# Performance work log

Measured on AMD Instinct MI355X. Metric: run time of the kernel, lower is better.

Reference implementation:

```python
import jax, jax.numpy as jnp
import numpy as np

# MiniCPM3 MLA attention dims
HIDDEN = 2560
N_HEADS = 40
Q_LORA = 768
KV_LORA = 256
ROPE_D = 32
NOPE_D = 64
V_D = HIDDEN // N_HEADS          # 64
Q_HEAD_D = NOPE_D + ROPE_D       # 96
ROPE_BASE = 10000.0
EPS = 1e-6


def setup_inputs() -> dict:
    key = jax.random.key(0)
    ks = jax.random.split(key, 8)
    B, S = 1, 2048
    sc = lambda fan_in: 1.0 / np.sqrt(fan_in)
    return {
        "hidden_states": jax.random.normal(ks[0], (B, S, HIDDEN), jnp.float32),
        "position_ids": jnp.arange(B * S, dtype=jnp.int64).reshape(B, S) % S,
        "w_qa": jax.random.normal(ks[1], (HIDDEN, Q_LORA), jnp.float32) * sc(HIDDEN),
        "q_a_ln_w": jnp.ones((Q_LORA,), jnp.float32),
        "w_qb": jax.random.normal(ks[2], (Q_LORA, N_HEADS * Q_HEAD_D), jnp.float32) * sc(Q_LORA),
        "w_kva": jax.random.normal(ks[3], (HIDDEN, KV_LORA + ROPE_D), jnp.float32) * sc(HIDDEN),
        "kv_a_ln_w": jnp.ones((KV_LORA,), jnp.float32),
        "w_kvb": jax.random.normal(ks[4], (KV_LORA, N_HEADS * (NOPE_D + V_D)), jnp.float32) * sc(KV_LORA),
        "w_o": jax.random.normal(ks[5], (N_HEADS * V_D, HIDDEN), jnp.float32) * sc(N_HEADS * V_D),
    }


def _rmsnorm(x, w, eps=EPS):
    var = jnp.mean(x * x, axis=-1, keepdims=True)
    return x * jax.lax.rsqrt(var + eps) * w


def _rotate_half(x):
    h = x.shape[-1] // 2
    return jnp.concatenate([-x[..., h:], x[..., :h]], axis=-1)


def _rope_cache(seq_len, dim, base, dtype=jnp.float32):
    inv_freq = 1.0 / (base ** (jnp.arange(0, dim, 2, dtype=jnp.float32) / dim))
    t = jnp.arange(seq_len, dtype=jnp.float32)
    freqs = jnp.outer(t, inv_freq)                      # [S, dim/2]
    emb = jnp.concatenate([freqs, freqs], axis=-1)      # [S, dim]
    return jnp.cos(emb).astype(dtype), jnp.sin(emb).astype(dtype)


def reference(hidden_states, position_ids, w_qa, q_a_ln_w, w_qb, w_kva, kv_a_ln_w, w_kvb, w_o):
    B, S, _ = hidden_states.shape
    # --- low-rank Q projection: a -> RMSNorm -> b ---
    q = _rmsnorm(hidden_states @ w_qa, q_a_ln_w) @ w_qb          # [B,S,H*96]
    q = q.reshape(B, S, N_HEADS, Q_HEAD_D).transpose(0, 2, 1, 3)  # [B,H,S,96]
    q_nope, q_pe = q[..., :NOPE_D], q[..., NOPE_D:]
    # --- compressed KV + shared rope key ---
    ckv = hidden_states @ w_kva                                   # [B,S,256+32]
    compressed_kv, k_pe = ckv[..., :KV_LORA], ckv[..., KV_LORA:]
    k_pe = k_pe[:, None, :, :]                                    # [B,1,S,32]
    kv = _rmsnorm(compressed_kv, kv_a_ln_w) @ w_kvb               # [B,S,H*(64+64)]
    kv = kv.reshape(B, S, N_HEADS, NOPE_D + V_D).transpose(0, 2, 1, 3)
    k_nope, v = kv[..., :NOPE_D], kv[..., NOPE_D:]                # [B,H,S,64] each
    # --- RoPE on the 32-dim rope sub-dimension (fp32, as original) ---
    cos, sin = _rope_cache(S, ROPE_D, ROPE_BASE)
    cos = cos[position_ids][:, None, :, :]                        # [B,1,S,32]
    sin = sin[position_ids][:, None, :, :]
    q_pe = q_pe * cos + _rotate_half(q_pe) * sin
    k_pe = k_pe * cos + _rotate_half(k_pe) * sin
    # --- concat nope/rope parts ---
    q_full = jnp.concatenate([q_nope, q_pe], axis=-1)             # [B,H,S,96]
    k_full = jnp.concatenate([k_nope, jnp.broadcast_to(k_pe, (B, N_HEADS, S, ROPE_D))], axis=-1)
    # --- causal SDPA with scale q_head_dim**-0.5 ---
    scale = Q_HEAD_D ** -0.5
    scores = jnp.einsum("bhqd,bhkd->bhqk", q_full, k_full) * scale
    causal = jnp.tril(jnp.ones((S, S), bool))
    scores = jnp.where(causal, scores, jnp.finfo(scores.dtype).min)
    probs = jax.nn.softmax(scores, axis=-1)
    attn = jnp.einsum("bhqk,bhkd->bhqd", probs, v)                # [B,H,S,64]
    attn = attn.transpose(0, 2, 1, 3).reshape(B, S, N_HEADS * V_D)
    return attn @ w_o
```

## Files before the change

kernel.cpp:

```cpp
#include <hip/hip_runtime.h>
#include <hip/hip_bf16.h>

typedef __hip_bfloat16 bf16;
typedef __attribute__((ext_vector_type(8))) __bf16 bf16x8;
typedef __attribute__((ext_vector_type(4))) __bf16 bf16x4;
typedef __attribute__((ext_vector_type(4))) float f32x4;

constexpr int S_LEN = 2048;
constexpr int HID   = 2560;
constexpr int NH    = 40;
constexpr int QL    = 768;
constexpr int KVL   = 256;
constexpr int RD    = 32;
constexpr int ND    = 64;
constexpr int VD    = 64;
constexpr int QHD   = 96;
constexpr int QB_N  = NH * QHD;
constexpr int KVB_N = NH * (ND + VD);
constexpr int CKV_N = KVL + RD;
constexpr int AB_N  = QL + CKV_N;

#define MFMA16(a, b, c) __builtin_amdgcn_mfma_f32_16x16x32_bf16((a), (b), (c), 0, 0, 0)

__device__ __forceinline__ int get_pos(const int* pos, int s) {
  bool is64 = (pos[1] == 0 && pos[2] == 1);
  return is64 ? pos[2 * s] : pos[s];
}


__global__ void cast_f32_bf16(const float* __restrict__ src, bf16* __restrict__ dst, int n4) {
  int i = blockIdx.x * blockDim.x + threadIdx.x;
  if (i >= n4) return;
  float4 v = reinterpret_cast<const float4*>(src)[i];
  struct { bf16 a, b, c, d; } pk;
  pk.a = __float2bfloat16(v.x); pk.b = __float2bfloat16(v.y);
  pk.c = __float2bfloat16(v.z); pk.d = __float2bfloat16(v.w);
  reinterpret_cast<uint2*>(dst)[i] = *reinterpret_cast<uint2*>(&pk);
}

__global__ void transpose_cast(const float* __restrict__ src, bf16* __restrict__ dst, int K, int N) {
  __shared__ float tile[32][33];
  int nb = blockIdx.x * 32, kb = blockIdx.y * 32;
  int x = threadIdx.x, y = threadIdx.y;
#pragma unroll
  for (int j = 0; j < 4; ++j) {
    int k = kb + y + j * 8, n = nb + x;
    tile[y + j * 8][x] = (k < K && n < N) ? src[(size_t)k * N + n] : 0.f;
  }
  __syncthreads();
#pragma unroll
  for (int j = 0; j < 4; ++j) {
    int n = nb + y + j * 8, k = kb + x;
    if (n < N && k < K) dst[(size_t)n * K + k] = __float2bfloat16(tile[x][y + j * 8]);
  }
}


__global__ __launch_bounds__(256) void gemm_qakva(const bf16* __restrict__ A,
                                                  const bf16* __restrict__ B,
                                                  float* __restrict__ q_out,
                                                  float* __restrict__ ckv_out) {
  constexpr int BM = 64, BK = 64, K = HID, N = AB_N;
  __shared__ __bf16 ldsA[BM * BK];
  __shared__ __bf16 ldsB[64 * BK];
  const int t = threadIdx.x;
  const int l = t & 63, w = t >> 6;
  const int lr = l & 15, lk = l >> 4;
  const int rowbase = blockIdx.y * BM;
  const int colbase = blockIdx.x * 64;

  f32x4 acc[4];
#pragma unroll
  for (int n = 0; n < 4; ++n) acc[n] = f32x4{0.f, 0.f, 0.f, 0.f};

  for (int kt = 0; kt < K / BK; ++kt) {
    const int kb = kt * BK;
#pragma unroll
    for (int it = 0; it < 2; ++it) {
      const int r  = it * 32 + w * 8 + (l >> 3);
      const int c8 = ((l & 7) * 8) ^ ((r & 7) << 3);
      const bf16* ga = A + (size_t)(rowbase + r) * K + kb + c8;
      __builtin_amdgcn_global_load_lds((const __attribute__((address_space(1))) void*)ga,
          (__attribute__((address_space(3))) void*)(ldsA + it * 2048 + w * 512), 16, 0, 0);
      int nrow = colbase + r;
      nrow = (nrow < N) ? nrow : (N - 1);
      const bf16* gb = B + (size_t)nrow * K + kb + c8;
      __builtin_amdgcn_global_load_lds((const __attribute__((address_space(1))) void*)gb,
          (__attribute__((address_space(3))) void*)(ldsB + it * 2048 + w * 512), 16, 0, 0);
    }
    __syncthreads();
#pragma unroll
    for (int kk = 0; kk < 2; ++kk) {
      const int arow = w * 16 + lr;
      const int ace  = (kk * 32 + lk * 8) ^ ((arow & 7) << 3);
      bf16x8 af = *(const bf16x8*)(ldsA + arow * BK + ace);
#pragma unroll
      for (int n = 0; n < 4; ++n) {
        const int row = n * 16 + lr;
        const int ce  = (kk * 32 + lk * 8) ^ ((row & 7) << 3);
        bf16x8 bfr = *(const bf16x8*)(ldsB + row * BK + ce);
        acc[n] = MFMA16(af, bfr, acc[n]);
      }
    }
    __syncthreads();
  }

#pragma unroll
  for (int n = 0; n < 4; ++n) {
    const int col = colbase + n * 16 + lr;
#pragma unroll
    for (int i = 0; i < 4; ++i) {
      const int row = rowbase + w * 16 + lk * 4 + i;
      if (col < QL)       q_out[(size_t)row * QL + col] = acc[n][i];
      else if (col < N)   ckv_out[(size_t)row * CKV_N + (col - QL)] = acc[n][i];
    }
  }
}

__global__ __launch_bounds__(256) void gemm_out64(const bf16* __restrict__ A,
                                                  const bf16* __restrict__ B,
                                                  float* __restrict__ C) {
  constexpr int BM = 128, BK = 64, K = HID, N = HID;
  __shared__ __bf16 ldsA[BM * BK];
  __shared__ __bf16 ldsB[64 * BK];
  const int t = threadIdx.x;
  const int l = t & 63, w = t >> 6;
  const int lr = l & 15, lk = l >> 4;
  const int rowbase = blockIdx.y * BM;
  const int colbase = blockIdx.x * 64;

  f32x4 acc[2][4];
#pragma unroll
  for (int m = 0; m < 2; ++m)
#pragma unroll
    for (int n = 0; n < 4; ++n) acc[m][n] = f32x4{0.f, 0.f, 0.f, 0.f};

  for (int kt = 0; kt < K / BK; ++kt) {
    const int kb = kt * BK;
#pragma unroll
    for (int it = 0; it < 4; ++it) {
      const int r  = it * 32 + w * 8 + (l >> 3);
      const int c8 = ((l & 7) * 8) ^ ((r & 7) << 3);
      const bf16* ga = A + (size_t)(rowbase + r) * K + kb + c8;
      __builtin_amdgcn_global_load_lds((const __attribute__((address_space(1))) void*)ga,
          (__attribute__((address_space(3))) void*)(ldsA + it * 2048 + w * 512), 16, 0, 0);
      if (it < 2) {
        const bf16* gb = B + (size_t)(colbase + r) * K + kb + c8;
        __builtin_amdgcn_global_load_lds((const __attribute__((address_space(1))) void*)gb,
            (__attribute__((address_space(3))) void*)(ldsB + it * 2048 + w * 512), 16, 0, 0);
      }
    }
    __syncthreads();
#pragma unroll
    for (int kk = 0; kk < 2; ++kk) {
      bf16x8 af[2], bfr[4];
#pragma unroll
      for (int m = 0; m < 2; ++m) {
        const int row = w * 32 + m * 16 + lr;
        const int ce  = (kk * 32 + lk * 8) ^ ((row & 7) << 3);
        af[m] = *(const bf16x8*)(ldsA + row * BK + ce);
      }
#pragma unroll
      for (int n = 0; n < 4; ++n) {
        const int row = n * 16 + lr;
        const int ce  = (kk * 32 + lk * 8) ^ ((row & 7) << 3);
        bfr[n] = *(const bf16x8*)(ldsB + row * BK + ce);
      }
#pragma unroll
      for (int m = 0; m < 2; ++m)
#pragma unroll
        for (int n = 0; n < 4; ++n)
          acc[m][n] = MFMA16(af[m], bfr[n], acc[m][n]);
    }
    __syncthreads();
  }

#pragma unroll
  for (int m = 0; m < 2; ++m)
#pragma unroll
    for (int n = 0; n < 4; ++n) {
      const int col = colbase + n * 16 + lr;
#pragma unroll
      for (int i = 0; i < 4; ++i) {
        const int row = rowbase + w * 32 + m * 16 + lk * 4 + i;
        C[(size_t)row * N + col] = acc[m][n][i];
      }
    }
}

__global__ __launch_bounds__(256) void gemm_qb_rope(const bf16* __restrict__ A,
                                                    const bf16* __restrict__ B,
                                                    const float* __restrict__ ropc,
                                                    const float* __restrict__ rops,
                                                    bf16* __restrict__ qfull) {
  constexpr int BM = 128, BK = 64, K = QL;
  __shared__ __bf16 ldsA[BM * BK];
  __shared__ __bf16 ldsB[64 * BK];
  const int t = threadIdx.x;
  const int l = t & 63, w = t >> 6;
  const int lr = l & 15, lk = l >> 4;
  const int rowbase = blockIdx.y * BM;
  const int colbase = blockIdx.x * 64;
  const float scale = 0.14724444f;

  f32x4 acc[2][4];
#pragma unroll
  for (int m = 0; m < 2; ++m)
#pragma unroll
    for (int n = 0; n < 4; ++n) acc[m][n] = f32x4{0.f, 0.f, 0.f, 0.f};

  for (int kt = 0; kt < K / BK; ++kt) {
    const int kb = kt * BK;
#pragma unroll
    for (int it = 0; it < 4; ++it) {
      const int r  = it * 32 + w * 8 + (l >> 3);
      const int c8 = ((l & 7) * 8) ^ ((r & 7) << 3);
      const bf16* ga = A + (size_t)(rowbase + r) * K + kb + c8;
      __builtin_amdgcn_global_load_lds((const __attribute__((address_space(1))) void*)ga,
          (__attribute__((address_space(3))) void*)(ldsA + it * 2048 + w * 512), 16, 0, 0);
      if (it < 2) {
        const bf16* gb = B + (size_t)(colbase + r) * K + kb + c8;
        __builtin_amdgcn_global_load_lds((const __attribute__((address_space(1))) void*)gb,
            (__attribute__((address_space(3))) void*)(ldsB + it * 2048 + w * 512), 16, 0, 0);
      }
    }
    __syncthreads();
#pragma unroll
    for (int kk = 0; kk < 2; ++kk) {
      bf16x8 af[2], bfr[4];
#pragma unroll
      for (int m = 0; m < 2; ++m) {
        const int row = w * 32 + m * 16 + lr;
        const int ce  = (kk * 32 + lk * 8) ^ ((row & 7) << 3);
        af[m] = *(const bf16x8*)(ldsA + row * BK + ce);
      }
#pragma unroll
      for (int n = 0; n < 4; ++n) {
        const int row = n * 16 + lr;
        const int ce  = (kk * 32 + lk * 8) ^ ((row & 7) << 3);
        bfr[n] = *(const bf16x8*)(ldsB + row * BK + ce);
      }
#pragma unroll
      for (int m = 0; m < 2; ++m)
#pragma unroll
        for (int n = 0; n < 4; ++n)
          acc[m][n] = MFMA16(af[m], bfr[n], acc[m][n]);
    }
    __syncthreads();
  }

#pragma unroll
  for (int m = 0; m < 2; ++m) {
    const int rowtop = rowbase + w * 32 + m * 16 + lk * 4;
#pragma unroll
    for (int n = 0; n < 4; ++n) {
      const int c0 = colbase + n * 16;
      const int h  = c0 / 96;
      const int d0 = c0 - h * 96;
      const size_t qb_ = ((size_t)h * S_LEN + rowtop) * QHD + d0 + lr;
      if (d0 < ND) {
#pragma unroll
        for (int i = 0; i < 4; ++i)
          qfull[qb_ + (size_t)i * QHD] = __float2bfloat16(acc[m][n][i] * scale);
      } else if (d0 == ND) {
#pragma unroll
        for (int i = 0; i < 4; ++i) {
          const float c = ropc[(rowtop + i) * 16 + lr];
          const float s = rops[(rowtop + i) * 16 + lr];
          const float x0 = acc[m][n][i], x1 = acc[m][n + 1][i];
          qfull[qb_ + (size_t)i * QHD] = __float2bfloat16((x0 * c - x1 * s) * scale);
        }
      } else {
#pragma unroll
        for (int i = 0; i < 4; ++i) {
          const float c = ropc[(rowtop + i) * 16 + lr];
          const float s = rops[(rowtop + i) * 16 + lr];
          const float x1 = acc[m][n][i], x0 = acc[m][n - 1][i];
          qfull[qb_ + (size_t)i * QHD] = __float2bfloat16((x1 * c + x0 * s) * scale);
        }
      }
    }
  }
}

__global__ __launch_bounds__(256) void gemm_kvb_split(const bf16* __restrict__ A,
                                                      const bf16* __restrict__ B,
                                                      bf16* __restrict__ kfull,
                                                      bf16* __restrict__ vt) {
  constexpr int BM = 128, BN = 128, BK = 64, K = KVL;
  __shared__ __bf16 ldsA[BM * BK];
  __shared__ __bf16 ldsB[BN * BK];
  const int t = threadIdx.x;
  const int l = t & 63, w = t >> 6;
  const int lr = l & 15, lk = l >> 4;
  const int wr = w >> 1, wc = w & 1;
  const int rowbase = blockIdx.y * BM;
  const int h = blockIdx.x;
  const int colbase = h * BN;

  f32x4 acc[4][4];
#pragma unroll
  for (int m = 0; m < 4; ++m)
#pragma unroll
    for (int n = 0; n < 4; ++n) acc[m][n] = f32x4{0.f, 0.f, 0.f, 0.f};

  for (int kt = 0; kt < K / BK; ++kt) {
    const int kb = kt * BK;
#pragma unroll
    for (int it = 0; it < 4; ++it) {
      const int r  = it * 32 + w * 8 + (l >> 3);
      const int c8 = ((l & 7) * 8) ^ ((r & 7) << 3);
      const bf16* ga = A + (size_t)(rowbase + r) * K + kb + c8;
      __builtin_amdgcn_global_load_lds((const __attribute__((address_space(1))) void*)ga,
          (__attribute__((address_space(3))) void*)(ldsA + it * 2048 + w * 512), 16, 0, 0);
      const bf16* gb = B + (size_t)(colbase + r) * K + kb + c8;
      __builtin_amdgcn_global_load_lds((const __attribute__((address_space(1))) void*)gb,
          (__attribute__((address_space(3))) void*)(ldsB + it * 2048 + w * 512), 16, 0, 0);
    }
    __syncthreads();
#pragma unroll
    for (int kk = 0; kk < 2; ++kk) {
      bf16x8 af[4], bfr[4];
#pragma unroll
      for (int m = 0; m < 4; ++m) {
        const int row = wr * 64 + m * 16 + lr;
        const int ce  = (kk * 32 + lk * 8) ^ ((row & 7) << 3);
        af[m] = *(const bf16x8*)(ldsA + row * BK + ce);
      }
#pragma unroll
      for (int n = 0; n < 4; ++n) {
        const int row = wc * 64 + n * 16 + lr;
        const int ce  = (kk * 32 + lk * 8) ^ ((row & 7) << 3);
        bfr[n] = *(const bf16x8*)(ldsB + row * BK + ce);
      }
#pragma unroll
      for (int m = 0; m < 4; ++m)
#pragma unroll
        for (int n = 0; n < 4; ++n)
          acc[m][n] = MFMA16(af[m], bfr[n], acc[m][n]);
    }
    __syncthreads();
  }

#pragma unroll
  for (int m = 0; m < 4; ++m) {
    const int rowtop = rowbase + wr * 64 + m * 16 + lk * 4;
    if (wc == 0) {
#pragma unroll
      for (int n = 0; n < 4; ++n) {
        const int d = n * 16 + lr;
#pragma unroll
        for (int i = 0; i < 4; ++i)
          kfull[((size_t)h * S_LEN + rowtop + i) * QHD + d] = __float2bfloat16(acc[m][n][i]);
      }
    } else {
#pragma unroll
      for (int n = 0; n < 4; ++n) {
        const int d = n * 16 + lr;
        bf16x4 pk;
#pragma unroll
        for (int i = 0; i < 4; ++i) pk[i] = (__bf16)acc[m][n][i];
        *(bf16x4*)(vt + ((size_t)h * VD + d) * S_LEN + rowtop) = pk;
      }
    }
  }
}


__global__ void rmsnorm_rows(const float* __restrict__ in, const float* __restrict__ w,
                             bf16* __restrict__ out, int C) {
  const int r = blockIdx.x;
  const float* row = in + (size_t)r * C;
  float ss = 0.f;
  for (int c = threadIdx.x; c < C; c += 256) { float v = row[c]; ss += v * v; }
#pragma unroll
  for (int d = 32; d > 0; d >>= 1) ss += __shfl_xor(ss, d);
  __shared__ float red[4];
  if ((threadIdx.x & 63) == 0) red[threadIdx.x >> 6] = ss;
  __syncthreads();
  const float tot = red[0] + red[1] + red[2] + red[3];
  const float rs = rsqrtf(tot / (float)C + 1e-6f);
  for (int c = threadIdx.x; c < C; c += 256)
    out[(size_t)r * C + c] = __float2bfloat16(row[c] * rs * w[c]);
}

__global__ void kv_prep(const float* __restrict__ ckv, const float* __restrict__ w,
                        const int* __restrict__ pos, bf16* __restrict__ ckv_bf,
                        bf16* __restrict__ kfull, float* __restrict__ ropc,
                        float* __restrict__ rops) {
  const int s = blockIdx.x, t = threadIdx.x;
  __shared__ bf16 pe_lds[32];
  const float* row = ckv + (size_t)s * CKV_N;
  float v[4]; float ss = 0.f;
#pragma unroll
  for (int j = 0; j < 4; ++j) { v[j] = row[t + 64 * j]; ss += v[j] * v[j]; }
#pragma unroll
  for (int d = 32; d > 0; d >>= 1) ss += __shfl_xor(ss, d);
  const float rs = rsqrtf(ss / (float)KVL + 1e-6f);
#pragma unroll
  for (int j = 0; j < 4; ++j)
    ckv_bf[(size_t)s * KVL + t + 64 * j] = __float2bfloat16(v[j] * rs * w[t + 64 * j]);
  if (t < 16) {
    const float x0 = row[KVL + t], x1 = row[KVL + 16 + t];
    const float p = (float)get_pos(pos, s);
    const float invf = exp2f(-(float)t * (13.2877124f / 16.f));
    const float ang = p * invf, c = cosf(ang), sn = sinf(ang);
    ropc[s * 16 + t] = c;
    rops[s * 16 + t] = sn;
    pe_lds[t]      = __float2bfloat16(x0 * c - x1 * sn);
    pe_lds[16 + t] = __float2bfloat16(x1 * c + x0 * sn);
  }
  __syncthreads();
  for (int idx = t; idx < NH * 32; idx += 64) {
    const int h = idx >> 5, d = idx & 31;
    kfull[((size_t)h * S_LEN + s) * QHD + ND + d] = pe_lds[d];
  }
}

__global__ __launch_bounds__(64) void attn_kernel(const bf16* __restrict__ qfull,
                                                  const bf16* __restrict__ kfull,
                                                  const bf16* __restrict__ vt,
                                                  bf16* __restrict__ ctx) {
  const int h = blockIdx.x;
  const int qw = ((int)gridDim.y - 1 - (int)blockIdx.y) * 32;
  const int l = threadIdx.x;
  const int lr = l & 15, lk = l >> 4;
  const bf16* Q  = qfull + (size_t)h * S_LEN * QHD;
  const bf16* Kf = kfull + (size_t)h * S_LEN * QHD;
  const bf16* V  = vt + (size_t)h * VD * S_LEN;
  __shared__ __bf16 plds[32][64];

  bf16x8 qf[2][3];
#pragma unroll
  for (int qg = 0; qg < 2; ++qg)
#pragma unroll
    for (int ks = 0; ks < 3; ++ks)
      qf[qg][ks] = *(const bf16x8*)(Q + (size_t)(qw + qg * 16 + lr) * QHD + ks * 32 + lk * 8);

  f32x4 o[2][4];
  float mrow[2], lrow[2];
#pragma unroll
  for (int qg = 0; qg < 2; ++qg) {
#pragma unroll
    for (int dt = 0; dt < 4; ++dt) o[qg][dt] = f32x4{0.f, 0.f, 0.f, 0.f};
    mrow[qg] = -1e30f; lrow[qg] = 0.f;
  }

  bf16x8 kf[4][3];
#pragma unroll
  for (int sub = 0; sub < 4; ++sub)
#pragma unroll
    for (int ks = 0; ks < 3; ++ks)
      kf[sub][ks] = *(const bf16x8*)(Kf + (size_t)(sub * 16 + lr) * QHD + ks * 32 + lk * 8);

  for (int kb = 0;; kb += 64) {
    bf16x8 vfr[2][4];
#pragma unroll
    for (int h2 = 0; h2 < 2; ++h2)
#pragma unroll
      for (int dt = 0; dt < 4; ++dt)
        vfr[h2][dt] = *(const bf16x8*)(V + (size_t)(dt * 16 + lr) * S_LEN + kb + h2 * 32 + lk * 8);

    f32x4 st[2][4];
#pragma unroll
    for (int qg = 0; qg < 2; ++qg)
#pragma unroll
      for (int sub = 0; sub < 4; ++sub) st[qg][sub] = f32x4{0.f, 0.f, 0.f, 0.f};
    __builtin_amdgcn_s_setprio(1);
#pragma unroll
    for (int qg = 0; qg < 2; ++qg)
#pragma unroll
      for (int sub = 0; sub < 4; ++sub)
#pragma unroll
        for (int ks = 0; ks < 3; ++ks)
          st[qg][sub] = MFMA16(kf[sub][ks], qf[qg][ks], st[qg][sub]);
    __builtin_amdgcn_s_setprio(0);

    const int nkb = kb + 64;
    if (nkb <= qw) {
#pragma unroll
      for (int sub = 0; sub < 4; ++sub)
#pragma unroll
        for (int ks = 0; ks < 3; ++ks)
          kf[sub][ks] = *(const bf16x8*)(Kf + (size_t)(nkb + sub * 16 + lr) * QHD + ks * 32 + lk * 8);
    }

    const bool diag = (kb + 64 > qw);
    float lmax[2];
#pragma unroll
    for (int qg = 0; qg < 2; ++qg) {
      const int q = qw + qg * 16 + lr;
      if (diag) {
#pragma unroll
        for (int sub = 0; sub < 4; ++sub)
#pragma unroll
          for (int i = 0; i < 4; ++i)
            if (kb + sub * 16 + lk * 4 + i > q) st[qg][sub][i] = -1e30f;
      }
      float m0 = -1e30f;
#pragma unroll
      for (int sub = 0; sub < 4; ++sub)
#pragma unroll
        for (int i = 0; i < 4; ++i) m0 = fmaxf(m0, st[qg][sub][i]);
      lmax[qg] = m0;
    }

    const bool noresc = __all((lmax[0] <= mrow[0] + 8.f) && (lmax[1] <= mrow[1] + 8.f));
    float mnew[2], fac[2];
    if (noresc) {
      mnew[0] = mrow[0]; mnew[1] = mrow[1];
    } else {
#pragma unroll
      for (int qg = 0; qg < 2; ++qg) {
        float t0 = lmax[qg];
        t0 = fmaxf(t0, __shfl_xor(t0, 16));
        t0 = fmaxf(t0, __shfl_xor(t0, 32));
        mnew[qg] = fmaxf(mrow[qg], t0);
        fac[qg] = exp2f(mrow[qg] - mnew[qg]);
        mrow[qg] = mnew[qg];
      }
    }

#pragma unroll
    for (int qg = 0; qg < 2; ++qg) {
      float ts = 0.f;
#pragma unroll
      for (int sub = 0; sub < 4; ++sub) {
        bf16x4 pk;
#pragma unroll
        for (int i = 0; i < 4; ++i) {
          const float p = exp2f(st[qg][sub][i] - mnew[qg]);
          ts += p;
          pk[i] = (__bf16)p;
        }
        const int swc = (sub * 16 + lk * 4) ^ ((lr & 7) << 3);
        *(bf16x4*)(&plds[qg * 16 + lr][swc]) = pk;
      }
      if (noresc) lrow[qg] += ts;
      else        lrow[qg] = lrow[qg] * fac[qg] + ts;
    }
    if (!noresc) {
#pragma unroll
      for (int qg = 0; qg < 2; ++qg)
#pragma unroll
        for (int i = 0; i < 4; ++i) {
          const float fr = __shfl(fac[qg], lk * 4 + i);
#pragma unroll
          for (int dt = 0; dt < 4; ++dt) o[qg][dt][i] *= fr;
        }
    }

#pragma unroll
    for (int h2 = 0; h2 < 2; ++h2) {
      const int swc = (h2 * 32 + lk * 8) ^ ((lr & 7) << 3);
      bf16x8 pa0 = *(const bf16x8*)(&plds[lr][swc]);
      bf16x8 pa1 = *(const bf16x8*)(&plds[16 + lr][swc]);
      __builtin_amdgcn_s_setprio(1);
#pragma unroll
      for (int dt = 0; dt < 4; ++dt) {
        o[0][dt] = MFMA16(pa0, vfr[h2][dt], o[0][dt]);
        o[1][dt] = MFMA16(pa1, vfr[h2][dt], o[1][dt]);
      }
      __builtin_amdgcn_s_setprio(0);
    }
    if (nkb > qw) break;
  }

#pragma unroll
  for (int qg = 0; qg < 2; ++qg) {
    float ls = lrow[qg];
    ls += __shfl_xor(ls, 16);
    ls += __shfl_xor(ls, 32);
    const float linv = 1.0f / ls;
#pragma unroll
    for (int i = 0; i < 4; ++i) {
      const float inv = __shfl(linv, lk * 4 + i);
#pragma unroll
      for (int dt = 0; dt < 4; ++dt) {
        const int row = qw + qg * 16 + lk * 4 + i;
        const int col = h * VD + dt * 16 + lr;
        ctx[(size_t)row * HID + col] = __float2bfloat16(o[qg][dt][i] * inv);
      }
    }
  }
}


extern "C" void kernel_launch(void* const* d_in, const int* in_sizes, int n_in,
                              void* d_out, int out_size, void* d_ws, size_t ws_size,
                              hipStream_t stream) {
  const float* hidden = (const float*)d_in[0];
  const int*   pos    = (const int*)d_in[1];
  const float* w_qa   = (const float*)d_in[2];
  const float* q_ln   = (const float*)d_in[3];
  const float* w_qb   = (const float*)d_in[4];
  const float* w_kva  = (const float*)d_in[5];
  const float* kv_ln  = (const float*)d_in[6];
  const float* w_kvb  = (const float*)d_in[7];
  const float* w_o    = (const float*)d_in[8];
  float* out = (float*)d_out;
  char* ws = (char*)d_ws;
  (void)in_sizes; (void)n_in; (void)out_size; (void)ws_size;

  size_t off = 0;
  auto take = [&](size_t bytes) -> char* {
    char* p = ws + off;
    off = (off + bytes + 255) & ~(size_t)255;
    return p;
  };
  bf16*  hid_bf = (bf16*)take((size_t)S_LEN * HID * 2);
  bf16*  wabT   = (bf16*)take((size_t)AB_N * HID * 2);
  bf16*  wqbT   = (bf16*)take((size_t)QB_N * QL * 2);
  bf16*  wkvbT  = (bf16*)take((size_t)KVB_N * KVL * 2);
  bf16*  woT    = (bf16*)take((size_t)HID * HID * 2);
  float* qlora  = (float*)take((size_t)S_LEN * QL * 4);
  bf16*  qa_bf  = (bf16*)take((size_t)S_LEN * QL * 2);
  bf16*  qfull  = (bf16*)take((size_t)NH * S_LEN * QHD * 2);
  float* ckv    = (float*)take((size_t)S_LEN * CKV_N * 4);
  bf16*  ckv_bf = (bf16*)take((size_t)S_LEN * KVL * 2);
  float* ropc   = (float*)take((size_t)S_LEN * 16 * 4);
  float* rops   = (float*)take((size_t)S_LEN * 16 * 4);
  bf16*  kfull  = (bf16*)take((size_t)NH * S_LEN * QHD * 2);
  bf16*  vt     = (bf16*)take((size_t)NH * VD * S_LEN * 2);
  bf16*  ctx    = (bf16*)take((size_t)S_LEN * HID * 2);

  const dim3 tb(32, 8);
  cast_f32_bf16<<<(S_LEN * HID / 4 + 255) / 256, 256, 0, stream>>>(hidden, hid_bf, S_LEN * HID / 4);
  transpose_cast<<<dim3((QL + 31) / 32, (HID + 31) / 32), tb, 0, stream>>>(w_qa, wabT, HID, QL);
  transpose_cast<<<dim3((CKV_N + 31) / 32, (HID + 31) / 32), tb, 0, stream>>>(w_kva, wabT + (size_t)QL * HID, HID, CKV_N);
  transpose_cast<<<dim3((QB_N + 31) / 32, (QL + 31) / 32), tb, 0, stream>>>(w_qb, wqbT, QL, QB_N);
  transpose_cast<<<dim3((KVB_N + 31) / 32, (KVL + 31) / 32), tb, 0, stream>>>(w_kvb, wkvbT, KVL, KVB_N);
  transpose_cast<<<dim3((HID + 31) / 32, (HID + 31) / 32), tb, 0, stream>>>(w_o, woT, HID, HID);

  gemm_qakva<<<dim3((AB_N + 63) / 64, S_LEN / 64), 256, 0, stream>>>(hid_bf, wabT, qlora, ckv);

  kv_prep<<<S_LEN, 64, 0, stream>>>(ckv, kv_ln, pos, ckv_bf, kfull, ropc, rops);

  rmsnorm_rows<<<S_LEN, 256, 0, stream>>>(qlora, q_ln, qa_bf, QL);
  gemm_qb_rope<<<dim3(QB_N / 64, S_LEN / 128), 256, 0, stream>>>(qa_bf, wqbT, ropc, rops, qfull);

  gemm_kvb_split<<<dim3(KVB_N / 128, S_LEN / 128), 256, 0, stream>>>(ckv_bf, wkvbT, kfull, vt);

  attn_kernel<<<dim3(NH, S_LEN / 32), 64, 0, stream>>>(qfull, kfull, vt, ctx);
  gemm_out64<<<dim3(HID / 64, S_LEN / 128), 256, 0, stream>>>(ctx, woT, out);
}
```

Measured before the change: 227.6 us.

## Split attention KV range across two waves with LDS softmax merge

Each attention block now runs two wavefronts. Each wave processes half of the causal KV tiles with its own online-softmax state, and the two partial results are merged through shared memory using max/sum rescaling. This is meant to shorten the serial KV loop per query tile and balance the causal workload, adding parallelism inside each block. The cost is extra LDS for the merge buffers, a barrier, and a merge epilogue. Query fragments are also loaded redundantly by both waves.

```diff
diff --git a/kernel.cpp b/kernel.cpp
--- a/kernel.cpp
+++ b/kernel.cpp
@@ -417,18 +417,27 @@
   }
 }
 
-__global__ __launch_bounds__(64) void attn_kernel(const bf16* __restrict__ qfull,
-                                                  const bf16* __restrict__ kfull,
-                                                  const bf16* __restrict__ vt,
-                                                  bf16* __restrict__ ctx) {
+__global__ __launch_bounds__(128) void attn_kernel(const bf16* __restrict__ qfull,
+                                                   const bf16* __restrict__ kfull,
+                                                   const bf16* __restrict__ vt,
+                                                   bf16* __restrict__ ctx) {
   const int h = blockIdx.x;
   const int qw = ((int)gridDim.y - 1 - (int)blockIdx.y) * 32;
-  const int l = threadIdx.x;
+  const int w = threadIdx.x >> 6;
+  const int l = threadIdx.x & 63;
   const int lr = l & 15, lk = l >> 4;
+  const int nt = (qw >> 6) + 1;
+  const int nA = (nt + 1) >> 1;
+  const int kb0    = (w == 0) ? 0 : nA * 64;
+  const int kbLast = (w == 0) ? (nA - 1) * 64 : (nt - 1) * 64;
+  const int diagkb = (nt - 1) * 64;
   const bf16* Q  = qfull + (size_t)h * S_LEN * QHD;
   const bf16* Kf = kfull + (size_t)h * S_LEN * QHD;
   const bf16* V  = vt + (size_t)h * VD * S_LEN;
-  __shared__ __bf16 plds[32][64];
+  __shared__ __bf16 plds[2][32][64];
+  __shared__ float cmbO[32][66];
+  __shared__ float lA_s[32];
+  __shared__ float mA_s[32];
 
   bf16x8 qf[2][3];
 #pragma unroll
@@ -446,140 +455,169 @@
     mrow[qg] = -1e30f; lrow[qg] = 0.f;
   }
 
-  bf16x8 kf[4][3];
-#pragma unroll
-  for (int sub = 0; sub < 4; ++sub)
-#pragma unroll
-    for (int ks = 0; ks < 3; ++ks)
-      kf[sub][ks] = *(const bf16x8*)(Kf + (size_t)(sub * 16 + lr) * QHD + ks * 32 + lk * 8);
-
-  for (int kb = 0;; kb += 64) {
-    bf16x8 vfr[2][4];
-#pragma unroll
-    for (int h2 = 0; h2 < 2; ++h2)
-#pragma unroll
-      for (int dt = 0; dt < 4; ++dt)
-        vfr[h2][dt] = *(const bf16x8*)(V + (size_t)(dt * 16 + lr) * S_LEN + kb + h2 * 32 + lk * 8);
-
-    f32x4 st[2][4];
-#pragma unroll
-    for (int qg = 0; qg < 2; ++qg)
-#pragma unroll
-      for (int sub = 0; sub < 4; ++sub) st[qg][sub] = f32x4{0.f, 0.f, 0.f, 0.f};
-    __builtin_amdgcn_s_setprio(1);
-#pragma unroll
-    for (int qg = 0; qg < 2; ++qg)
-#pragma unroll
-      for (int sub = 0; sub < 4; ++sub)
-#pragma unroll
-        for (int ks = 0; ks < 3; ++ks)
-          st[qg][sub] = MFMA16(kf[sub][ks], qf[qg][ks], st[qg][sub]);
-    __builtin_amdgcn_s_setprio(0);
-
-    const int nkb = kb + 64;
-    if (nkb <= qw) {
-#pragma unroll
-      for (int sub = 0; sub < 4; ++sub)
-#pragma unroll
-        for (int ks = 0; ks < 3; ++ks)
-          kf[sub][ks] = *(const bf16x8*)(Kf + (size_t)(nkb + sub * 16 + lr) * QHD + ks * 32 + lk * 8);
-    }
-
-    const bool diag = (kb + 64 > qw);
-    float lmax[2];
+  if (kb0 <= kbLast) {
+    bf16x8 kf[4][3];
+#pragma unroll
+    for (int sub = 0; sub < 4; ++sub)
+#pragma unroll
+      for (int ks = 0; ks < 3; ++ks)
+        kf[sub][ks] = *(const bf16x8*)(Kf + (size_t)(kb0 + sub * 16 + lr) * QHD + ks * 32 + lk * 8);
+
+    for (int kb = kb0; kb <= kbLast; kb += 64) {
+      bf16x8 vfr[2][4];
+#pragma unroll
+      for (int h2 = 0; h2 < 2; ++h2)
+#pragma unroll
+        for (int dt = 0; dt < 4; ++dt)
+          vfr[h2][dt] = *(const bf16x8*)(V + (size_t)(dt * 16 + lr) * S_LEN + kb + h2 * 32 + lk * 8);
+
+      f32x4 st[2][4];
+#pragma unroll
+      for (int qg = 0; qg < 2; ++qg)
+#pragma unroll
+        for (int sub = 0; sub < 4; ++sub) st[qg][sub] = f32x4{0.f, 0.f, 0.f, 0.f};
+      __builtin_amdgcn_s_setprio(1);
+#pragma unroll
+      for (int qg = 0; qg < 2; ++qg)
+#pragma unroll
+        for (int sub = 0; sub < 4; ++sub)
+#pragma unroll
+          for (int ks = 0; ks < 3; ++ks)
+            st[qg][sub] = MFMA16(kf[sub][ks], qf[qg][ks], st[qg][sub]);
+      __builtin_amdgcn_s_setprio(0);
+
+      const int nkb = kb + 64;
+      if (nkb <= kbLast) {
+#pragma unroll
+        for (int sub = 0; sub < 4; ++sub)
+#pragma unroll
+          for (int ks = 0; ks < 3; ++ks)
+            kf[sub][ks] = *(const bf16x8*)(Kf + (size_t)(nkb + sub * 16 + lr) * QHD + ks * 32 + lk * 8);
+      }
+
+      float lmax[2];
+#pragma unroll
+      for (int qg = 0; qg < 2; ++qg) {
+        const int q = qw + qg * 16 + lr;
+        if (kb == diagkb) {
+#pragma unroll
+          for (int sub = 0; sub < 4; ++sub)
+#pragma unroll
+            for (int i = 0; i < 4; ++i)
+              if (kb + sub * 16 + lk * 4 + i > q) st[qg][sub][i] = -1e30f;
+        }
+        float m0 = -1e30f;
+#pragma unroll
+        for (int sub = 0; sub < 4; ++sub)
+#pragma unroll
+          for (int i = 0; i < 4; ++i) m0 = fmaxf(m0, st[qg][sub][i]);
+        lmax[qg] = m0;
+      }
+
+      const bool noresc = __all((lmax[0] <= mrow[0] + 8.f) && (lmax[1] <= mrow[1] + 8.f));
+      float mnew[2], fac[2];
+      if (noresc) {
+        mnew[0] = mrow[0]; mnew[1] = mrow[1];
+      } else {
+#pragma unroll
+        for (int qg = 0; qg < 2; ++qg) {
+          float t0 = lmax[qg];
+          t0 = fmaxf(t0, __shfl_xor(t0, 16));
+          t0 = fmaxf(t0, __shfl_xor(t0, 32));
+          mnew[qg] = fmaxf(mrow[qg], t0);
+          fac[qg] = exp2f(mrow[qg] - mnew[qg]);
+          mrow[qg] = mnew[qg];
+        }
+      }
+
+#pragma unroll
+      for (int qg = 0; qg < 2; ++qg) {
+        float ts = 0.f;
+#pragma unroll
+        for (int sub = 0; sub < 4; ++sub) {
+          bf16x4 pk;
+#pragma unroll
+          for (int i = 0; i < 4; ++i) {
+            const float p = exp2f(st[qg][sub][i] - mnew[qg]);
+            ts += p;
+            pk[i] = (__bf16)p;
+          }
+          const int swc = (sub * 16 + lk * 4) ^ ((lr & 7) << 3);
+          *(bf16x4*)(&plds[w][qg * 16 + lr][swc]) = pk;
+        }
+        if (noresc) lrow[qg] += ts;
+        else        lrow[qg] = lrow[qg] * fac[qg] + ts;
+      }
+      if (!noresc) {
+#pragma unroll
+        for (int qg = 0; qg < 2; ++qg)
+#pragma unroll
+          for (int i = 0; i < 4; ++i) {
+            const float fr = __shfl(fac[qg], lk * 4 + i);
+#pragma unroll
+            for (int dt = 0; dt < 4; ++dt) o[qg][dt][i] *= fr;
+          }
+      }
+
+#pragma unroll
+      for (int h2 = 0; h2 < 2; ++h2) {
+        const int swc = (h2 * 32 + lk * 8) ^ ((lr & 7) << 3);
+        bf16x8 pa0 = *(const bf16x8*)(&plds[w][lr][swc]);
+        bf16x8 pa1 = *(const bf16x8*)(&plds[w][16 + lr][swc]);
+        __builtin_amdgcn_s_setprio(1);
+#pragma unroll
+        for (int dt = 0; dt < 4; ++dt) {
+          o[0][dt] = MFMA16(pa0, vfr[h2][dt], o[0][dt]);
+          o[1][dt] = MFMA16(pa1, vfr[h2][dt], o[1][dt]);
+        }
+        __builtin_amdgcn_s_setprio(0);
+      }
+    }
+  }
+
+  float ls[2];
+#pragma unroll
+  for (int qg = 0; qg < 2; ++qg) {
+    float v = lrow[qg];
+    v += __shfl_xor(v, 16);
+    v += __shfl_xor(v, 32);
+    ls[qg] = v;
+  }
+
+  if (w == 0) {
 #pragma unroll
     for (int qg = 0; qg < 2; ++qg) {
-      const int q = qw + qg * 16 + lr;
-      if (diag) {
-#pragma unroll
-        for (int sub = 0; sub < 4; ++sub)
-#pragma unroll
-          for (int i = 0; i < 4; ++i)
-            if (kb + sub * 16 + lk * 4 + i > q) st[qg][sub][i] = -1e30f;
-      }
-      float m0 = -1e30f;
-#pragma unroll
-      for (int sub = 0; sub < 4; ++sub)
-#pragma unroll
-        for (int i = 0; i < 4; ++i) m0 = fmaxf(m0, st[qg][sub][i]);
-      lmax[qg] = m0;
-    }
-
-    const bool noresc = __all((lmax[0] <= mrow[0] + 8.f) && (lmax[1] <= mrow[1] + 8.f));
-    float mnew[2], fac[2];
-    if (noresc) {
-      mnew[0] = mrow[0]; mnew[1] = mrow[1];
-    } else {
-#pragma unroll
-      for (int qg = 0; qg < 2; ++qg) {
-        float t0 = lmax[qg];
-        t0 = fmaxf(t0, __shfl_xor(t0, 16));
-        t0 = fmaxf(t0, __shfl_xor(t0, 32));
-        mnew[qg] = fmaxf(mrow[qg], t0);
-        fac[qg] = exp2f(mrow[qg] - mnew[qg]);
-        mrow[qg] = mnew[qg];
-      }
-    }
-
+#pragma unroll
+      for (int i = 0; i < 4; ++i)
+#pragma unroll
+        for (int dt = 0; dt < 4; ++dt)
+          cmbO[qg * 16 + lk * 4 + i][dt * 16 + lr] = o[qg][dt][i];
+      if (lk == 0) {
+        lA_s[qg * 16 + lr] = ls[qg];
+        mA_s[qg * 16 + lr] = mrow[qg];
+      }
+    }
+  }
+  __syncthreads();
+  if (w == 1) {
 #pragma unroll
     for (int qg = 0; qg < 2; ++qg) {
-      float ts = 0.f;
-#pragma unroll
-      for (int sub = 0; sub < 4; ++sub) {
-        bf16x4 pk;
-#pragma unroll
-        for (int i = 0; i < 4; ++i) {
-          const float p = exp2f(st[qg][sub][i] - mnew[qg]);
-          ts += p;
-          pk[i] = (__bf16)p;
+#pragma unroll
+      for (int i = 0; i < 4; ++i) {
+        const int r16 = qg * 16 + lk * 4 + i;
+        const float mB = __shfl(mrow[qg], lk * 4 + i);
+        const float lB = __shfl(ls[qg],   lk * 4 + i);
+        const float mA = mA_s[r16];
+        const float M  = fmaxf(mA, mB);
+        const float wAf = exp2f(mA - M);
+        const float wBf = exp2f(mB - M);
+        const float inv = 1.0f / (wAf * lA_s[r16] + wBf * lB);
+        const int row = qw + r16;
+#pragma unroll
+        for (int dt = 0; dt < 4; ++dt) {
+          const float vv = (wAf * cmbO[r16][dt * 16 + lr] + wBf * o[qg][dt][i]) * inv;
+          ctx[(size_t)row * HID + h * VD + dt * 16 + lr] = __float2bfloat16(vv);
         }
-        const int swc = (sub * 16 + lk * 4) ^ ((lr & 7) << 3);
-        *(bf16x4*)(&plds[qg * 16 + lr][swc]) = pk;
-      }
-      if (noresc) lrow[qg] += ts;
-      else        lrow[qg] = lrow[qg] * fac[qg] + ts;
-    }
-    if (!noresc) {
-#pragma unroll
-      for (int qg = 0; qg < 2; ++qg)
-#pragma unroll
-        for (int i = 0; i < 4; ++i) {
-          const float fr = __shfl(fac[qg], lk * 4 + i);
-#pragma unroll
-          for (int dt = 0; dt < 4; ++dt) o[qg][dt][i] *= fr;
-        }
-    }
-
-#pragma unroll
-    for (int h2 = 0; h2 < 2; ++h2) {
-      const int swc = (h2 * 32 + lk * 8) ^ ((lr & 7) << 3);
-      bf16x8 pa0 = *(const bf16x8*)(&plds[lr][swc]);
-      bf16x8 pa1 = *(const bf16x8*)(&plds[16 + lr][swc]);
-      __builtin_amdgcn_s_setprio(1);
-#pragma unroll
-      for (int dt = 0; dt < 4; ++dt) {
-        o[0][dt] = MFMA16(pa0, vfr[h2][dt], o[0][dt]);
-        o[1][dt] = MFMA16(pa1, vfr[h2][dt], o[1][dt]);
-      }
-      __builtin_amdgcn_s_setprio(0);
-    }
-    if (nkb > qw) break;
-  }
-
-#pragma unroll
-  for (int qg = 0; qg < 2; ++qg) {
-    float ls = lrow[qg];
-    ls += __shfl_xor(ls, 16);
-    ls += __shfl_xor(ls, 32);
-    const float linv = 1.0f / ls;
-#pragma unroll
-    for (int i = 0; i < 4; ++i) {
-      const float inv = __shfl(linv, lk * 4 + i);
-#pragma unroll
-      for (int dt = 0; dt < 4; ++dt) {
-        const int row = qw + qg * 16 + lk * 4 + i;
-        const int col = h * VD + dt * 16 + lr;
-        ctx[(size_t)row * HID + col] = __float2bfloat16(o[qg][dt][i] * inv);
       }
     }
   }
@@ -641,6 +679,6 @@
 
   gemm_kvb_split<<<dim3(KVB_N / 128, S_LEN / 128), 256, 0, stream>>>(ckv_bf, wkvbT, kfull, vt);
 
-  attn_kernel<<<dim3(NH, S_LEN / 32), 64, 0, stream>>>(qfull, kfull, vt, ctx);
+  attn_kernel<<<dim3(NH, S_LEN / 32), 128, 0, stream>>>(qfull, kfull, vt, ctx);
   gemm_out64<<<dim3(HID / 64, S_LEN / 128), 256, 0, stream>>>(ctx, woT, out);
 }
```

Result: no change. 230.2 us (+1.1%).
